# Kernel optimization log

Measured on AMD Instinct MI355X. Metric: run time of the kernel, lower is better.

## Reference

```python
import jax, jax.numpy as jnp
import numpy as np
from jax import lax


def binarize(x):
    # sign() binarization with straight-through estimator (identity backward),
    # matching the BNN .data in-place trick in BinarizeConv2d / bilinear.
    return x + lax.stop_gradient(jnp.sign(x) - x)


def maxpool2x2(x):
    # NCHW 2x2 max pool, stride 2
    return lax.reduce_window(x, -jnp.inf, lax.max,
                             (1, 1, 2, 2), (1, 1, 2, 2), 'VALID')


def conv2d(x, w):
    # NCHW / OIHW valid conv, stride 1
    return lax.conv_general_dilated(x, w, (1, 1), 'VALID',
                                    dimension_numbers=('NCHW', 'OIHW', 'NCHW'))


def setup_inputs() -> dict:
    key = jax.random.key(0)
    ks = jax.random.split(key, 6)
    B = 16384
    x = jax.random.normal(ks[0], (B, 1, 32, 32), dtype=jnp.float32)
    w1 = jax.random.normal(ks[1], (6, 1, 5, 5), dtype=jnp.float32) * 0.2
    w2 = jax.random.normal(ks[2], (16, 6, 5, 5), dtype=jnp.float32) * 0.08
    wfc1 = jax.random.normal(ks[3], (120, 400), dtype=jnp.float32) * 0.05
    wfc2 = jax.random.normal(ks[4], (84, 120), dtype=jnp.float32) * 0.09
    wfc3 = jax.random.normal(ks[5], (10, 84), dtype=jnp.float32) * 0.1
    return {'x': x, 'w1': w1, 'w2': w2, 'wfc1': wfc1, 'wfc2': wfc2, 'wfc3': wfc3}


def reference(x, w1, w2, wfc1, wfc2, wfc3):
    # conv1 (binarized input + weights) -> pool
    h = maxpool2x2(conv2d(binarize(x), binarize(w1)))          # [B,6,14,14]
    # conv2 -> pool
    h = maxpool2x2(conv2d(binarize(h), binarize(w2)))          # [B,16,5,5]
    h = h.reshape(h.shape[0], -1)                              # [B,400]
    h = binarize(h) @ binarize(wfc1).T                         # [B,120]
    h = binarize(h) @ binarize(wfc2).T                         # [B,84]
    h = binarize(h) @ binarize(wfc3).T                         # [B,10]
    return h
```

## Files before the change

kernel.cpp:

```cpp
#include <hip/hip_runtime.h>
#include <hip/hip_bf16.h>

typedef unsigned int u32;
typedef unsigned long long u64;

#define OC1 0
#define OC2 8
#define WCONV 104
#define OF1 104
#define OF2 2024
#define OF3 2664
#define WTOT 2704

__global__ void pack_w(const float* __restrict__ w1, const float* __restrict__ w2,
                       const float* __restrict__ f1, const float* __restrict__ f2,
                       const float* __restrict__ f3, u64* __restrict__ P) {
    int g = blockIdx.x * 256 + threadIdx.x;
    if (g < 1920) {
        int j = g / 15, w = g % 15;
        u64 v = 0;
        if (w < 14 && j < 120) {
            bool sp = (w >= 7); int k = sp ? w - 7 : w;
            for (int f = 0; f < 4; f++) {
                int p = 4 * k + f;
                if (p < 25)
                    for (int ch = 0; ch < 16; ch++) {
                        float x = f1[j * 400 + ch * 25 + p];
                        bool b = sp ? (x < 0.0f) : (x != 0.0f);
                        if (b) v |= 1ull << (f * 16 + ch);
                    }
            }
        }
        P[OF1 + g] = v;
    } else if (g < 2560) {
        int g2 = g - 1920, j = g2 / 5, w = g2 % 5;
        u64 v = 0;
        if (w < 4 && j < 84) {
            bool sp = (w >= 2); int h = w & 1;
            for (int b = 0; b < 64; b++) {
                int k = h * 64 + b;
                if (k < 120) {
                    float x = f2[j * 120 + k];
                    bool bb = sp ? (x < 0.0f) : (x != 0.0f);
                    if (bb) v |= 1ull << b;
                }
            }
        }
        P[OF2 + g2] = v;
    } else if (g < 2600) {
        int g3 = g - 2560, j = g3 / 4, w = g3 % 4;
        bool sp = (w >= 2); int h = w & 1;
        u64 v = 0;
        for (int b = 0; b < 64; b++) {
            int k = h * 64 + b;
            if (k < 84) {
                float x = f3[j * 84 + k];
                bool bb = sp ? (x < 0.0f) : (x != 0.0f);
                if (bb) v |= 1ull << b;
            }
        }
        P[OF3 + g3] = v;
    } else if (g < 2696) {
        int c = g - 2600, ch = c / 6, w = c % 6;
        bool sp = (w >= 3); int wp = w % 3;
        u64 v = 0;
        for (int half = 0; half < 2; half++) {
            int r = 2 * wp + half;
            if (r < 5) {
                u32 rowv = 0;
                for (int ci = 0; ci < 6; ci++)
                    for (int cc = 0; cc < 5; cc++) {
                        float x = w2[((ch * 6 + ci) * 5 + r) * 5 + cc];
                        bool b = sp ? (x < 0.0f) : (x != 0.0f);
                        int bit = (ci < 3) ? (5 * ci + cc) : (15 + 5 * (ci - 3) + cc);
                        if (b) rowv |= 1u << bit;
                    }
                v |= (u64)rowv << (32 * half);
            }
        }
        P[OC2 + ch * 6 + (sp ? 3 : 0) + wp] = v;
    } else if (g < 2702) {
        int c = g - 2696;
        int pair = c % 3; bool sp = (c >= 3);
        u64 v = 0;
        for (int half = 0; half < 2; half++) {
            int ch = 2 * pair + half;
            u32 wd = 0;
            for (int r = 0; r < 5; r++)
                for (int cc = 0; cc < 5; cc++) {
                    float x = w1[ch * 25 + r * 5 + cc];
                    bool b = sp ? (x < 0.0f) : (x != 0.0f);
                    if (b) wd |= 1u << (6 * r + cc);
                }
            v |= (u64)wd << (32 * half);
        }
        P[OC1 + (sp ? 3 : 0) + pair] = v;
    }
}

#define G 8

__device__ __forceinline__ u32 sgnb(int v) { return (u32)v >> 31; }
__device__ __forceinline__ u32 nzb(int v)  { return (u32)(v | -v) >> 31; }

__global__ __launch_bounds__(256, 8) void lenet_main(const float* __restrict__ X,
                                                     const u64* __restrict__ P,
                                                     float* __restrict__ out) {
    __shared__ u64 WL[WCONV];
    __shared__ u32 xs[G][32], xn[G][32];
    __shared__ u64 h1An[G][14], h1As[G][14], h1Bn[G][14], h1Bs[G][14];
    __shared__ u64 h2n[G][7], h2s[G][7];
    __shared__ u64 f1s[G][2], f1n[G][2], f2s[G][2], f2n[G][2];
    __shared__ u32 anyz, dirty;

    const int tid = threadIdx.x;
    const int img0 = blockIdx.x * G;

    if (tid < WCONV) WL[tid] = P[tid];
    if (tid < G * 7) { int im = tid / 7, k = tid % 7; h2n[im][k] = 0; h2s[im][k] = 0; }
    if (tid == 0) { anyz = 0; dirty = 0; }
    __syncthreads();

    if (tid < 51) {
        u64 w, exp;
        if (tid < 48) {
            int ch = tid / 3, k = tid % 3;
            w = WL[OC2 + ch * 6 + k];
            exp = (k < 2) ? 0x3FFFFFFF3FFFFFFFull : 0x000000003FFFFFFFull;
        } else {
            w = WL[OC1 + (tid - 48)];
            exp = 0x1F7DF7DF1F7DF7DFull;
        }
        if (w != exp) dirty = 1;
    }

    {
        const float4* X4 = (const float4*)(X + (size_t)img0 * 1024);
        for (int it = 0; it < G; it++) {
            float4 v = X4[it * 256 + tid];
            u32 s = (v.x < 0.0f ? 1u : 0u) | (v.y < 0.0f ? 2u : 0u)
                  | (v.z < 0.0f ? 4u : 0u) | (v.w < 0.0f ? 8u : 0u);
            u32 n = (v.x != 0.0f ? 1u : 0u) | (v.y != 0.0f ? 2u : 0u)
                  | (v.z != 0.0f ? 4u : 0u) | (v.w != 0.0f ? 8u : 0u);
            if (n != 15u) anyz = 1;
            int pos = 4 * (tid & 7);
            u32 sw = s << pos, nw = n << pos;
            sw |= __shfl_xor((int)sw, 1); sw |= __shfl_xor((int)sw, 2); sw |= __shfl_xor((int)sw, 4);
            nw |= __shfl_xor((int)nw, 1); nw |= __shfl_xor((int)nw, 2); nw |= __shfl_xor((int)nw, 4);
            if ((tid & 7) == 0) { xs[it][tid >> 3] = sw; xn[it][tid >> 3] = nw; }
        }
    }
    __syncthreads();

    const bool fastp = ((anyz | dirty) == 0);

    {
        const int px = tid & 15;
        const int pxe = px < 14 ? px : 13;
        if (fastp) {
            u64 c1s[3];
            for (int p = 0; p < 3; p++) c1s[p] = WL[OC1 + 3 + p];
            for (int it = 0; it < 7; it++) {
                int seg = it * 16 + (tid >> 4);
                int img = seg / 14, py = seg % 14;
                int oy = 2 * py;
                u32 rs[6];
                for (int k = 0; k < 6; k++) rs[k] = xs[img][oy + k];
                u32 cnt[6];
                for (int c = 0; c < 6; c++) cnt[c] = 255;
                for (int dx = 0; dx < 2; dx++) {
                    int t2 = 2 * pxe + dx;
                    u32 w0 = 0;
                    for (int r = 0; r < 5; r++) w0 |= ((rs[r] >> t2) & 31u) << (6 * r);
                    u32 w1 = (w0 >> 6) | (((rs[5] >> t2) & 31u) << 24);
                    for (int dy = 0; dy < 2; dy++) {
                        u32 w = dy ? w1 : w0;
                        u64 W = ((u64)w << 32) | w;
                        for (int p = 0; p < 3; p++) {
                            u64 t = W ^ c1s[p];
                            cnt[2 * p]     = min(cnt[2 * p],     (u32)__popc((u32)t));
                            cnt[2 * p + 1] = min(cnt[2 * p + 1], (u32)__popc((u32)(t >> 32)));
                        }
                    }
                }
                u64 bS[6];
                for (int c = 0; c < 6; c++) bS[c] = __ballot(cnt[c] >= 13);
                if (px == 0) {
                    int sh = tid & 48;
                    u64 rAs = ((bS[0] >> sh) & 0x3FFF) | (((bS[1] >> sh) & 0x3FFF) << 16) | (((bS[2] >> sh) & 0x3FFF) << 32);
                    u64 rBs = ((bS[3] >> sh) & 0x3FFF) | (((bS[4] >> sh) & 0x3FFF) << 16) | (((bS[5] >> sh) & 0x3FFF) << 32);
                    h1As[img][py] = rAs; h1Bs[img][py] = rBs;
                }
            }
        } else {
            u64 c1n[3], c1s[3];
            for (int p = 0; p < 3; p++) { c1n[p] = WL[OC1 + p]; c1s[p] = WL[OC1 + 3 + p]; }
            for (int it = 0; it < 7; it++) {
                int seg = it * 16 + (tid >> 4);
                int img = seg / 14, py = seg % 14;
                int oy = 2 * py;
                u32 rn[6], rs[6];
                for (int k = 0; k < 6; k++) { rn[k] = xn[img][oy + k]; rs[k] = xs[img][oy + k]; }
                int best[6];
                for (int c = 0; c < 6; c++) best[c] = -1000;
                for (int dx = 0; dx < 2; dx++) {
                    int t2 = 2 * pxe + dx;
                    u32 wn0 = 0, ws0 = 0;
                    for (int r = 0; r < 5; r++) {
                        wn0 |= ((rn[r] >> t2) & 31u) << (6 * r);
                        ws0 |= ((rs[r] >> t2) & 31u) << (6 * r);
                    }
                    u32 wn1 = (wn0 >> 6) | (((rn[5] >> t2) & 31u) << 24);
                    u32 ws1 = (ws0 >> 6) | (((rs[5] >> t2) & 31u) << 24);
                    for (int dy = 0; dy < 2; dy++) {
                        u32 wn = dy ? wn1 : wn0, ws = dy ? ws1 : ws0;
                        u64 Wn = ((u64)wn << 32) | wn;
                        u64 Ws = ((u64)ws << 32) | ws;
                        for (int p = 0; p < 3; p++) {
                            u64 m  = Wn & c1n[p];
                            u64 mx = m & (Ws ^ c1s[p]);
                            int a0 = __popc((u32)m) - 2 * __popc((u32)mx);
                            int a1 = __popc((u32)(m >> 32)) - 2 * __popc((u32)(mx >> 32));
                            best[2 * p]     = max(best[2 * p], a0);
                            best[2 * p + 1] = max(best[2 * p + 1], a1);
                        }
                    }
                }
                u64 bS[6], bN[6];
                for (int c = 0; c < 6; c++) {
                    bS[c] = __ballot(best[c] < 0);
                    bN[c] = __ballot(best[c] != 0);
                }
                if (px == 0) {
                    int sh = tid & 48;
                    u64 rAs = ((bS[0] >> sh) & 0x3FFF) | (((bS[1] >> sh) & 0x3FFF) << 16) | (((bS[2] >> sh) & 0x3FFF) << 32);
                    u64 rAn = ((bN[0] >> sh) & 0x3FFF) | (((bN[1] >> sh) & 0x3FFF) << 16) | (((bN[2] >> sh) & 0x3FFF) << 32);
                    u64 rBs = ((bS[3] >> sh) & 0x3FFF) | (((bS[4] >> sh) & 0x3FFF) << 16) | (((bS[5] >> sh) & 0x3FFF) << 32);
                    u64 rBn = ((bN[3] >> sh) & 0x3FFF) | (((bN[4] >> sh) & 0x3FFF) << 16) | (((bN[5] >> sh) & 0x3FFF) << 32);
                    h1As[img][py] = rAs; h1An[img][py] = rAn;
                    h1Bs[img][py] = rBs; h1Bn[img][py] = rBn;
                }
            }
        }
    }
    __syncthreads();

    if (fastp) {
        for (int idx = tid; idx < G * 25; idx += 256) {
            int img = idx / 25, p = idx % 25, py = p / 5, px = p % 5;
            int y0 = 2 * py;
            u32 dsg[2][6];
            for (int r = 0; r < 6; r++) {
                u64 a = h1As[img][y0 + r], b = h1Bs[img][y0 + r];
                for (int dx = 0; dx < 2; dx++) {
                    int t2 = 2 * px + dx;
                    u64 as = a >> t2, bs = b >> t2;
                    dsg[dx][r] = (((u32)as & 31u) | ((u32)(as >> 11) & 0x3E0u) | ((u32)(as >> 22) & 0x7C00u))
                               | ((((u32)bs & 31u) | ((u32)(bs >> 11) & 0x3E0u) | ((u32)(bs >> 22) & 0x7C00u)) << 15);
                }
            }
            u64 Ps[2][4];
            for (int dx = 0; dx < 2; dx++)
                for (int r = 0; r < 4; r++)
                    Ps[dx][r] = (u64)dsg[dx][r] | ((u64)dsg[dx][r + 1] << 32);
            u64 sb = 0, nb = 0;
            for (int ch = 0; ch < 16; ch++) {
                u64 w0s = WL[OC2 + ch * 6 + 3], w1s = WL[OC2 + ch * 6 + 4];
                u32 w2s = (u32)WL[OC2 + ch * 6 + 5];
                u32 mn = 255;
                for (int dy = 0; dy < 2; dy++)
                    for (int dx = 0; dx < 2; dx++) {
                        u64 t0 = Ps[dx][dy] ^ w0s, t1 = Ps[dx][dy + 2] ^ w1s;
                        u32 t2v = (dy ? dsg[dx][5] : dsg[dx][4]) ^ w2s;
                        u32 c = __popcll(t0) + __popcll(t1) + __popc(t2v);
                        mn = min(mn, c);
                    }
                sb |= (u64)(mn >= 76 ? 1 : 0) << ch;
                nb |= (u64)(mn != 75 ? 1 : 0) << ch;
            }
            int k = p >> 2, f = p & 3;
            atomicOr(&h2s[img][k], sb << (16 * f));
            atomicOr(&h2n[img][k], nb << (16 * f));
        }
    } else {
        for (int idx = tid; idx < G * 25; idx += 256) {
            int img = idx / 25, p = idx % 25, py = p / 5, px = p % 5;
            int y0 = 2 * py;
            u32 dn[2][6], dsg[2][6];
            for (int r = 0; r < 6; r++) {
                u64 a_n = h1An[img][y0 + r], a_s = h1As[img][y0 + r];
                u64 b_n = h1Bn[img][y0 + r], b_s = h1Bs[img][y0 + r];
                for (int dx = 0; dx < 2; dx++) {
                    int t2 = 2 * px + dx;
                    u64 an = a_n >> t2, as = a_s >> t2, bn = b_n >> t2, bs = b_s >> t2;
                    dn[dx][r]  = (((u32)an & 31u) | ((u32)(an >> 11) & 0x3E0u) | ((u32)(an >> 22) & 0x7C00u))
                               | ((((u32)bn & 31u) | ((u32)(bn >> 11) & 0x3E0u) | ((u32)(bn >> 22) & 0x7C00u)) << 15);
                    dsg[dx][r] = (((u32)as & 31u) | ((u32)(as >> 11) & 0x3E0u) | ((u32)(as >> 22) & 0x7C00u))
                               | ((((u32)bs & 31u) | ((u32)(bs >> 11) & 0x3E0u) | ((u32)(bs >> 22) & 0x7C00u)) << 15);
                }
            }
            u64 Pn[2][4], Ps[2][4];
            for (int dx = 0; dx < 2; dx++)
                for (int r = 0; r < 4; r++) {
                    Pn[dx][r] = (u64)dn[dx][r]  | ((u64)dn[dx][r + 1]  << 32);
                    Ps[dx][r] = (u64)dsg[dx][r] | ((u64)dsg[dx][r + 1] << 32);
                }
            u64 sb = 0, nb = 0;
            for (int ch = 0; ch < 16; ch++) {
                const u64* wp = &WL[OC2 + ch * 6];
                u64 w0n = wp[0], w1n = wp[1]; u32 w2n = (u32)wp[2];
                u64 w0s = wp[3], w1s = wp[4]; u32 w2s = (u32)wp[5];
                int am = -1000000;
                for (int dy = 0; dy < 2; dy++)
                    for (int dx = 0; dx < 2; dx++) {
                        u64 m0 = Pn[dx][dy] & w0n, m1 = Pn[dx][dy + 2] & w1n;
                        u32 m2 = (dy ? dn[dx][5] : dn[dx][4]) & w2n;
                        u64 x0 = m0 & (Ps[dx][dy] ^ w0s), x1 = m1 & (Ps[dx][dy + 2] ^ w1s);
                        u32 x2 = m2 & ((dy ? dsg[dx][5] : dsg[dx][4]) ^ w2s);
                        int v = __popcll(m0) + __popcll(m1) + __popc(m2)
                              - 2 * (__popcll(x0) + __popcll(x1) + __popc(x2));
                        am = max(am, v);
                    }
                sb |= (u64)sgnb(am) << ch;
                nb |= (u64)nzb(am) << ch;
            }
            int k = p >> 2, f = p & 3;
            atomicOr(&h2s[img][k], sb << (16 * f));
            atomicOr(&h2n[img][k], nb << (16 * f));
        }
    }
    __syncthreads();

    for (int r = 0; r < G / 2; r++) {
        int slot = r * 256 + tid;
        int img = slot >> 7, j = slot & 127, word = (slot >> 6) & 1;
        const u64* wj = P + OF1 + j * 15;
        int acc = 0;
        for (int k = 0; k < 7; k++) {
            u64 m  = h2n[img][k] & wj[k];
            u64 mx = m & (h2s[img][k] ^ wj[7 + k]);
            acc += __popcll(m) - 2 * __popcll(mx);
        }
        u64 bs = __ballot(acc < 0);
        u64 bn = __ballot(acc != 0);
        if ((tid & 63) == 0) { f1s[img][word] = bs; f1n[img][word] = bn; }
    }
    __syncthreads();

    for (int r = 0; r < G / 2; r++) {
        int slot = r * 256 + tid;
        int img = slot >> 7, j = slot & 127, word = (slot >> 6) & 1;
        const u64* wj = P + OF2 + j * 5;
        u64 m0 = f1n[img][0] & wj[0], m1 = f1n[img][1] & wj[1];
        u64 x0 = m0 & (f1s[img][0] ^ wj[2]), x1 = m1 & (f1s[img][1] ^ wj[3]);
        int acc = __popcll(m0) + __popcll(m1) - 2 * (__popcll(x0) + __popcll(x1));
        u64 bs = __ballot(acc < 0);
        u64 bn = __ballot(acc != 0);
        if ((tid & 63) == 0) { f2s[img][word] = bs; f2n[img][word] = bn; }
    }
    __syncthreads();

    if (tid < G * 16) {
        int img = tid >> 4, j = tid & 15;
        if (j < 10) {
            const u64* wj = P + OF3 + j * 4;
            u64 m0 = f2n[img][0] & wj[0], m1 = f2n[img][1] & wj[1];
            u64 x0 = m0 & (f2s[img][0] ^ wj[2]), x1 = m1 & (f2s[img][1] ^ wj[3]);
            int acc = __popcll(m0) + __popcll(m1) - 2 * (__popcll(x0) + __popcll(x1));
            out[(size_t)(img0 + img) * 10 + j] = (float)acc;
        }
    }
}

extern "C" void kernel_launch(void* const* d_in, const int* in_sizes, int n_in,
                              void* d_out, int out_size, void* d_ws, size_t ws_size,
                              hipStream_t stream) {
    const float* x    = (const float*)d_in[0];
    const float* w1   = (const float*)d_in[1];
    const float* w2   = (const float*)d_in[2];
    const float* wfc1 = (const float*)d_in[3];
    const float* wfc2 = (const float*)d_in[4];
    const float* wfc3 = (const float*)d_in[5];
    float* out = (float*)d_out;
    u64* P = (u64*)d_ws;

    int B = in_sizes[0] / 1024;

    pack_w<<<11, 256, 0, stream>>>(w1, w2, wfc1, wfc2, wfc3, P);
    lenet_main<<<B / G, 256, 0, stream>>>(x, P, out);
}
```

Baseline: 148.3 us.

## Assign two images per wavefront and replace block barriers with wave barriers

Each 64-lane wavefront now owns two images end to end: it loads their pixels, checks the zero and weight flags via ballots, and runs conv1, conv2 and the FC layers on them. The block-wide __syncthreads between stages become wave barriers, and the shared anyz/dirty flags become per-wave ballots. This removes cross-wave synchronization stalls so waves can progress independently. In exchange some stages use only part of the wave (conv2 uses 50 of 64 lanes), the weight-flag check is repeated in every wave from global memory, and correctness now relies on wave-level LDS ordering.

```diff
diff --git a/kernel.cpp b/kernel.cpp
--- a/kernel.cpp
+++ b/kernel.cpp
@@ -102,6 +102,7 @@
 
 __device__ __forceinline__ u32 sgnb(int v) { return (u32)v >> 31; }
 __device__ __forceinline__ u32 nzb(int v)  { return (u32)(v | -v) >> 31; }
+#define WB() __builtin_amdgcn_wave_barrier()
 
 __global__ __launch_bounds__(256, 8) void lenet_main(const float* __restrict__ X,
                                                      const u64* __restrict__ P,
@@ -111,61 +112,66 @@
     __shared__ u64 h1An[G][14], h1As[G][14], h1Bn[G][14], h1Bs[G][14];
     __shared__ u64 h2n[G][7], h2s[G][7];
     __shared__ u64 f1s[G][2], f1n[G][2], f2s[G][2], f2n[G][2];
-    __shared__ u32 anyz, dirty;
 
     const int tid = threadIdx.x;
+    const int wid = tid >> 6, lane = tid & 63;
     const int img0 = blockIdx.x * G;
+    const int li0 = wid * 2;
 
     if (tid < WCONV) WL[tid] = P[tid];
-    if (tid < G * 7) { int im = tid / 7, k = tid % 7; h2n[im][k] = 0; h2s[im][k] = 0; }
-    if (tid == 0) { anyz = 0; dirty = 0; }
     __syncthreads();
 
-    if (tid < 51) {
-        u64 w, exp;
-        if (tid < 48) {
-            int ch = tid / 3, k = tid % 3;
-            w = WL[OC2 + ch * 6 + k];
-            exp = (k < 2) ? 0x3FFFFFFF3FFFFFFFull : 0x000000003FFFFFFFull;
-        } else {
-            w = WL[OC1 + (tid - 48)];
-            exp = 0x1F7DF7DF1F7DF7DFull;
-        }
-        if (w != exp) dirty = 1;
-    }
-
+    u64 zb = 0;
     {
         const float4* X4 = (const float4*)(X + (size_t)img0 * 1024);
-        for (int it = 0; it < G; it++) {
-            float4 v = X4[it * 256 + tid];
+        for (int it = 0; it < 8; it++) {
+            int li = li0 + (it >> 2);
+            int f4 = ((it & 3) << 6) + lane;
+            float4 v = X4[li * 256 + f4];
             u32 s = (v.x < 0.0f ? 1u : 0u) | (v.y < 0.0f ? 2u : 0u)
                   | (v.z < 0.0f ? 4u : 0u) | (v.w < 0.0f ? 8u : 0u);
             u32 n = (v.x != 0.0f ? 1u : 0u) | (v.y != 0.0f ? 2u : 0u)
                   | (v.z != 0.0f ? 4u : 0u) | (v.w != 0.0f ? 8u : 0u);
-            if (n != 15u) anyz = 1;
-            int pos = 4 * (tid & 7);
+            zb |= __ballot(n != 15u);
+            int pos = 4 * (f4 & 7);
             u32 sw = s << pos, nw = n << pos;
             sw |= __shfl_xor((int)sw, 1); sw |= __shfl_xor((int)sw, 2); sw |= __shfl_xor((int)sw, 4);
             nw |= __shfl_xor((int)nw, 1); nw |= __shfl_xor((int)nw, 2); nw |= __shfl_xor((int)nw, 4);
-            if ((tid & 7) == 0) { xs[it][tid >> 3] = sw; xn[it][tid >> 3] = nw; }
-        }
-    }
-    __syncthreads();
-
-    const bool fastp = ((anyz | dirty) == 0);
-
+            if ((lane & 7) == 0) { xs[li][f4 >> 3] = sw; xn[li][f4 >> 3] = nw; }
+        }
+    }
+    u64 db;
     {
-        const int px = tid & 15;
+        bool bad = false;
+        if (lane < 51) {
+            u64 w, exp;
+            if (lane < 48) {
+                int ch = lane / 3, k = lane % 3;
+                w = P[OC2 + ch * 6 + k];
+                exp = (k < 2) ? 0x3FFFFFFF3FFFFFFFull : 0x000000003FFFFFFFull;
+            } else {
+                w = P[OC1 + (lane - 48)];
+                exp = 0x1F7DF7DF1F7DF7DFull;
+            }
+            bad = (w != exp);
+        }
+        db = __ballot(bad);
+    }
+    const bool fastp = ((zb | db) == 0);
+    WB();
+
+    {
+        const int px = lane & 15;
         const int pxe = px < 14 ? px : 13;
         if (fastp) {
             u64 c1s[3];
             for (int p = 0; p < 3; p++) c1s[p] = WL[OC1 + 3 + p];
             for (int it = 0; it < 7; it++) {
-                int seg = it * 16 + (tid >> 4);
-                int img = seg / 14, py = seg % 14;
+                int seg = it * 4 + (lane >> 4);
+                int im = seg >= 14 ? 1 : 0, py = seg - 14 * im, li = li0 + im;
                 int oy = 2 * py;
                 u32 rs[6];
-                for (int k = 0; k < 6; k++) rs[k] = xs[img][oy + k];
+                for (int k = 0; k < 6; k++) rs[k] = xs[li][oy + k];
                 u32 cnt[6];
                 for (int c = 0; c < 6; c++) cnt[c] = 255;
                 for (int dx = 0; dx < 2; dx++) {
@@ -186,21 +192,21 @@
                 u64 bS[6];
                 for (int c = 0; c < 6; c++) bS[c] = __ballot(cnt[c] >= 13);
                 if (px == 0) {
-                    int sh = tid & 48;
+                    int sh = lane & 48;
                     u64 rAs = ((bS[0] >> sh) & 0x3FFF) | (((bS[1] >> sh) & 0x3FFF) << 16) | (((bS[2] >> sh) & 0x3FFF) << 32);
                     u64 rBs = ((bS[3] >> sh) & 0x3FFF) | (((bS[4] >> sh) & 0x3FFF) << 16) | (((bS[5] >> sh) & 0x3FFF) << 32);
-                    h1As[img][py] = rAs; h1Bs[img][py] = rBs;
+                    h1As[li][py] = rAs; h1Bs[li][py] = rBs;
                 }
             }
         } else {
             u64 c1n[3], c1s[3];
             for (int p = 0; p < 3; p++) { c1n[p] = WL[OC1 + p]; c1s[p] = WL[OC1 + 3 + p]; }
             for (int it = 0; it < 7; it++) {
-                int seg = it * 16 + (tid >> 4);
-                int img = seg / 14, py = seg % 14;
+                int seg = it * 4 + (lane >> 4);
+                int im = seg >= 14 ? 1 : 0, py = seg - 14 * im, li = li0 + im;
                 int oy = 2 * py;
                 u32 rn[6], rs[6];
-                for (int k = 0; k < 6; k++) { rn[k] = xn[img][oy + k]; rs[k] = xs[img][oy + k]; }
+                for (int k = 0; k < 6; k++) { rn[k] = xn[li][oy + k]; rs[k] = xs[li][oy + k]; }
                 int best[6];
                 for (int c = 0; c < 6; c++) best[c] = -1000;
                 for (int dx = 0; dx < 2; dx++) {
@@ -232,28 +238,30 @@
                     bN[c] = __ballot(best[c] != 0);
                 }
                 if (px == 0) {
-                    int sh = tid & 48;
+                    int sh = lane & 48;
                     u64 rAs = ((bS[0] >> sh) & 0x3FFF) | (((bS[1] >> sh) & 0x3FFF) << 16) | (((bS[2] >> sh) & 0x3FFF) << 32);
                     u64 rAn = ((bN[0] >> sh) & 0x3FFF) | (((bN[1] >> sh) & 0x3FFF) << 16) | (((bN[2] >> sh) & 0x3FFF) << 32);
                     u64 rBs = ((bS[3] >> sh) & 0x3FFF) | (((bS[4] >> sh) & 0x3FFF) << 16) | (((bS[5] >> sh) & 0x3FFF) << 32);
                     u64 rBn = ((bN[3] >> sh) & 0x3FFF) | (((bN[4] >> sh) & 0x3FFF) << 16) | (((bN[5] >> sh) & 0x3FFF) << 32);
-                    h1As[img][py] = rAs; h1An[img][py] = rAn;
-                    h1Bs[img][py] = rBs; h1Bn[img][py] = rBn;
-                }
-            }
-        }
-    }
-    __syncthreads();
-
+                    h1As[li][py] = rAs; h1An[li][py] = rAn;
+                    h1Bs[li][py] = rBs; h1Bn[li][py] = rBn;
+                }
+            }
+        }
+    }
+    WB();
+
+    if (lane < 14) { int li = li0 + (lane >= 7 ? 1 : 0); int k = lane % 7; h2n[li][k] = 0; h2s[li][k] = 0; }
     if (fastp) {
-        for (int idx = tid; idx < G * 25; idx += 256) {
-            int img = idx / 25, p = idx % 25, py = p / 5, px = p % 5;
+        if (lane < 50) {
+            int im = lane >= 25 ? 1 : 0, p = lane - 25 * im, li = li0 + im;
+            int py = p / 5, px2 = p % 5;
             int y0 = 2 * py;
             u32 dsg[2][6];
             for (int r = 0; r < 6; r++) {
-                u64 a = h1As[img][y0 + r], b = h1Bs[img][y0 + r];
+                u64 a = h1As[li][y0 + r], b = h1Bs[li][y0 + r];
                 for (int dx = 0; dx < 2; dx++) {
-                    int t2 = 2 * px + dx;
+                    int t2 = 2 * px2 + dx;
                     u64 as = a >> t2, bs = b >> t2;
                     dsg[dx][r] = (((u32)as & 31u) | ((u32)(as >> 11) & 0x3E0u) | ((u32)(as >> 22) & 0x7C00u))
                                | ((((u32)bs & 31u) | ((u32)(bs >> 11) & 0x3E0u) | ((u32)(bs >> 22) & 0x7C00u)) << 15);
@@ -279,19 +287,20 @@
                 nb |= (u64)(mn != 75 ? 1 : 0) << ch;
             }
             int k = p >> 2, f = p & 3;
-            atomicOr(&h2s[img][k], sb << (16 * f));
-            atomicOr(&h2n[img][k], nb << (16 * f));
+            atomicOr(&h2s[li][k], sb << (16 * f));
+            atomicOr(&h2n[li][k], nb << (16 * f));
         }
     } else {
-        for (int idx = tid; idx < G * 25; idx += 256) {
-            int img = idx / 25, p = idx % 25, py = p / 5, px = p % 5;
+        if (lane < 50) {
+            int im = lane >= 25 ? 1 : 0, p = lane - 25 * im, li = li0 + im;
+            int py = p / 5, px2 = p % 5;
             int y0 = 2 * py;
             u32 dn[2][6], dsg[2][6];
             for (int r = 0; r < 6; r++) {
-                u64 a_n = h1An[img][y0 + r], a_s = h1As[img][y0 + r];
-                u64 b_n = h1Bn[img][y0 + r], b_s = h1Bs[img][y0 + r];
+                u64 a_n = h1An[li][y0 + r], a_s = h1As[li][y0 + r];
+                u64 b_n = h1Bn[li][y0 + r], b_s = h1Bs[li][y0 + r];
                 for (int dx = 0; dx < 2; dx++) {
-                    int t2 = 2 * px + dx;
+                    int t2 = 2 * px2 + dx;
                     u64 an = a_n >> t2, as = a_s >> t2, bn = b_n >> t2, bs = b_s >> t2;
                     dn[dx][r]  = (((u32)an & 31u) | ((u32)(an >> 11) & 0x3E0u) | ((u32)(an >> 22) & 0x7C00u))
                                | ((((u32)bn & 31u) | ((u32)(bn >> 11) & 0x3E0u) | ((u32)(bn >> 22) & 0x7C00u)) << 15);
@@ -325,49 +334,49 @@
                 nb |= (u64)nzb(am) << ch;
             }
             int k = p >> 2, f = p & 3;
-            atomicOr(&h2s[img][k], sb << (16 * f));
-            atomicOr(&h2n[img][k], nb << (16 * f));
-        }
-    }
-    __syncthreads();
-
-    for (int r = 0; r < G / 2; r++) {
-        int slot = r * 256 + tid;
-        int img = slot >> 7, j = slot & 127, word = (slot >> 6) & 1;
+            atomicOr(&h2s[li][k], sb << (16 * f));
+            atomicOr(&h2n[li][k], nb << (16 * f));
+        }
+    }
+    WB();
+
+    for (int it = 0; it < 4; it++) {
+        int im = it >> 1, word = it & 1, li = li0 + im;
+        int j = word * 64 + lane;
         const u64* wj = P + OF1 + j * 15;
         int acc = 0;
         for (int k = 0; k < 7; k++) {
-            u64 m  = h2n[img][k] & wj[k];
-            u64 mx = m & (h2s[img][k] ^ wj[7 + k]);
+            u64 m  = h2n[li][k] & wj[k];
+            u64 mx = m & (h2s[li][k] ^ wj[7 + k]);
             acc += __popcll(m) - 2 * __popcll(mx);
         }
         u64 bs = __ballot(acc < 0);
         u64 bn = __ballot(acc != 0);
-        if ((tid & 63) == 0) { f1s[img][word] = bs; f1n[img][word] = bn; }
-    }
-    __syncthreads();
-
-    for (int r = 0; r < G / 2; r++) {
-        int slot = r * 256 + tid;
-        int img = slot >> 7, j = slot & 127, word = (slot >> 6) & 1;
+        if (lane == 0) { f1s[li][word] = bs; f1n[li][word] = bn; }
+    }
+    WB();
+
+    for (int it = 0; it < 4; it++) {
+        int im = it >> 1, word = it & 1, li = li0 + im;
+        int j = word * 64 + lane;
         const u64* wj = P + OF2 + j * 5;
-        u64 m0 = f1n[img][0] & wj[0], m1 = f1n[img][1] & wj[1];
-        u64 x0 = m0 & (f1s[img][0] ^ wj[2]), x1 = m1 & (f1s[img][1] ^ wj[3]);
+        u64 m0 = f1n[li][0] & wj[0], m1 = f1n[li][1] & wj[1];
+        u64 x0 = m0 & (f1s[li][0] ^ wj[2]), x1 = m1 & (f1s[li][1] ^ wj[3]);
         int acc = __popcll(m0) + __popcll(m1) - 2 * (__popcll(x0) + __popcll(x1));
         u64 bs = __ballot(acc < 0);
         u64 bn = __ballot(acc != 0);
-        if ((tid & 63) == 0) { f2s[img][word] = bs; f2n[img][word] = bn; }
-    }
-    __syncthreads();
-
-    if (tid < G * 16) {
-        int img = tid >> 4, j = tid & 15;
+        if (lane == 0) { f2s[li][word] = bs; f2n[li][word] = bn; }
+    }
+    WB();
+
+    if (lane < 32) {
+        int im = lane >> 4, j = lane & 15, li = li0 + im;
         if (j < 10) {
             const u64* wj = P + OF3 + j * 4;
-            u64 m0 = f2n[img][0] & wj[0], m1 = f2n[img][1] & wj[1];
-            u64 x0 = m0 & (f2s[img][0] ^ wj[2]), x1 = m1 & (f2s[img][1] ^ wj[3]);
+            u64 m0 = f2n[li][0] & wj[0], m1 = f2n[li][1] & wj[1];
+            u64 x0 = m0 & (f2s[li][0] ^ wj[2]), x1 = m1 & (f2s[li][1] ^ wj[3]);
             int acc = __popcll(m0) + __popcll(m1) - 2 * (__popcll(x0) + __popcll(x1));
-            out[(size_t)(img0 + img) * 10 + j] = (float)acc;
+            out[(size_t)(img0 + li) * 10 + j] = (float)acc;
         }
     }
 }
```

Result: no change. 148.2 us (-0.0%).
